# Kernel tuning notes

Hardware: AMD Instinct MI355X
Metric: run time of the kernel (lower is better)

The kernel has to match this reference:

```python
import jax, jax.numpy as jnp
import numpy as np

N = 100000
E = 3200000
F_IN = 256
F_OUT = 256
HID = 64


def setup_inputs() -> dict:
    key = jax.random.key(0)
    ks = jax.random.split(key, 16)
    stdv = 1.0 / np.sqrt(F_OUT)
    std_att = 1.0 / np.sqrt(HID)
    std_att_vec = 1.0 / np.sqrt(3.0)
    u = lambda k, shape, s: jax.random.uniform(k, shape, jnp.float32, -s, s)
    return {
        "inputx": jax.random.normal(ks[0], (N, F_IN), jnp.float32),
        "row_A": jax.random.randint(ks[1], (E,), 0, N),
        "col_A": jax.random.randint(ks[2], (E,), 0, N),
        "val_A": jax.random.uniform(ks[3], (E,), jnp.float32),
        "row_A2": jax.random.randint(ks[4], (E,), 0, N),
        "col_A2": jax.random.randint(ks[5], (E,), 0, N),
        "val_A2": jax.random.uniform(ks[6], (E,), jnp.float32),
        "weight_A": u(ks[7], (F_IN, F_OUT), stdv),
        "weight_A2": u(ks[8], (F_IN, F_OUT), stdv),
        "weight_mlp": u(ks[9], (F_IN, F_OUT), stdv),
        "W_k0": u(ks[10], (F_OUT, HID), std_att),
        "W_k1": u(ks[11], (F_OUT, HID), std_att),
        "W_k2": u(ks[12], (F_OUT, HID), std_att),
        "att_vec_A": u(ks[13], (F_OUT, HID), std_att),
        "att_vec_A2": u(ks[14], (F_OUT, HID), std_att),
        "att_vec_mlp": u(ks[15], (F_OUT, HID), std_att),
        "att_vec": u(jax.random.fold_in(key, 99), (3, 3), std_att_vec),
    }


def _spmm(row, col, val, x, n):
    # COO sparse-dense matmul: out[r] += val_e * x[c]
    return jax.ops.segment_sum(val[:, None] * x[col], row, num_segments=n)


def reference(inputx, row_A, col_A, val_A, row_A2, col_A2, val_A2,
              weight_A, weight_A2, weight_mlp, W_k0, W_k1, W_k2,
              att_vec_A, att_vec_A2, att_vec_mlp, att_vec):
    n = inputx.shape[0]
    out_A = jax.nn.relu(_spmm(row_A, col_A, val_A, inputx @ weight_A, n))
    out_A2 = jax.nn.relu(_spmm(row_A2, col_A2, val_A2, inputx @ weight_A2, n))
    out_mlp = jax.nn.relu(inputx @ weight_mlp)
    # attention gating
    T = 3.0
    k0 = jnp.mean(out_A @ W_k0, axis=0, keepdims=True)    # [1, HID]
    k1 = jnp.mean(out_A2 @ W_k1, axis=0, keepdims=True)
    k2 = jnp.mean(out_mlp @ W_k2, axis=0, keepdims=True)
    logits = jnp.concatenate([
        (out_A @ att_vec_A) @ k0.T,      # [N, 1]
        (out_A2 @ att_vec_A2) @ k1.T,
        (out_mlp @ att_vec_mlp) @ k2.T,
    ], axis=1)                           # [N, 3]
    att = jax.nn.softmax((jax.nn.sigmoid(logits) @ att_vec) / T, axis=1)
    return 3.0 * (att[:, 0:1] * out_A + att[:, 1:2] * out_A2 + att[:, 2:3] * out_mlp)
```

## Files before the change

### kernel.cpp

```cpp
#include <hip/hip_runtime.h>

typedef __bf16 bf16;
typedef __bf16 bf16x4 __attribute__((ext_vector_type(4)));
typedef __bf16 bf16x8 __attribute__((ext_vector_type(8)));
typedef float f32x4 __attribute__((ext_vector_type(4)));

__device__ __forceinline__ f32x4 bf2f(bf16x4 v){
  f32x4 r; r[0]=(float)v[0]; r[1]=(float)v[1]; r[2]=(float)v[2]; r[3]=(float)v[3]; return r;
}

#define RB    256
#define NBMAX 400
#define NBP   401
#define CHUNK 8192
#define CAP   9216

__global__ __launch_bounds__(256) void k_xcvt(const float* __restrict__ X, bf16* __restrict__ Xb, int total){
  int i = (blockIdx.x*256 + threadIdx.x)*8;
  if (i + 8 <= total){
    float4 a = *(const float4*)(X+i);
    float4 b = *(const float4*)(X+i+4);
    bf16x8 v;
    v[0]=(bf16)a.x; v[1]=(bf16)a.y; v[2]=(bf16)a.z; v[3]=(bf16)a.w;
    v[4]=(bf16)b.x; v[5]=(bf16)b.y; v[6]=(bf16)b.z; v[7]=(bf16)b.w;
    *(bf16x8*)(Xb+i) = v;
  }
}

__global__ __launch_bounds__(256) void k_wt(const float* __restrict__ W0, const float* __restrict__ W1,
                                            const float* __restrict__ W2, bf16* __restrict__ WT3){
  int n = blockIdx.x, mat = blockIdx.y, k = threadIdx.x;
  const float* W = (mat==0)?W0:((mat==1)?W1:W2);
  WT3[mat*65536 + n*256 + k] = (bf16)W[k*256 + n];
}

__global__ __launch_bounds__(512) void k_binT(const int* __restrict__ rowA, const int* __restrict__ colA,
    const float* __restrict__ valA, const int* __restrict__ rowA2, const int* __restrict__ colA2,
    const float* __restrict__ valA2, int* __restrict__ gcur,
    int2* __restrict__ pTA, int2* __restrict__ pTA2, int E, int NB){
  __shared__ int hist[NBMAX];
  __shared__ int lstart[NBMAX];
  __shared__ int delta[NBMAX];
  __shared__ int ss[512];
  __shared__ unsigned short sidx[CHUNK];
  __shared__ unsigned short bop[CHUNK];
  int mat = blockIdx.y;
  const int* row = mat? rowA2 : rowA;
  const int* col = mat? colA2 : colA;
  const float* val = mat? valA2 : valA;
  int2* pT = mat? pTA2 : pTA;
  int t = threadIdx.x;
  for (int i=t; i<NB; i+=512) hist[i] = 0;
  __syncthreads();
  int base = blockIdx.x * CHUNK;
  int endi = base + CHUNK; if (endi > E) endi = E;
  int cnt = endi - base;
  for (int i = base + t; i < endi; i += 512) atomicAdd(&hist[row[i] >> 8], 1);
  __syncthreads();
  int v = (t < NB) ? hist[t] : 0;
  ss[t] = v; __syncthreads();
  for (int off=1; off<512; off<<=1){
    int u = (t>=off)? ss[t-off] : 0;
    __syncthreads();
    ss[t] += u;
    __syncthreads();
  }
  if (t < NB){
    int excl = ss[t] - v;
    lstart[t] = excl;
    int ofs = v ? atomicAdd(&gcur[mat*NB + t], v) : 0;
    if (ofs > CAP - v) ofs = (CAP - v > 0) ? CAP - v : 0;
    delta[t] = (t*CAP + ofs) - excl;
    hist[t] = 0;
  }
  __syncthreads();
  for (int i = base + t; i < endi; i += 512){
    int b = row[i] >> 8;
    int lpos = lstart[b] + atomicAdd(&hist[b], 1);
    sidx[lpos] = (unsigned short)(i - base);
    bop[lpos]  = (unsigned short)b;
  }
  __syncthreads();
  for (int j = t; j < cnt; j += 512){
    int i = base + (int)sidx[j];
    int b = bop[j];
    int r = row[i];
    int2 p; p.x = ((r & 255) << 17) | col[i]; p.y = __float_as_int(val[i]);
    pT[delta[b] + j] = p;
  }
}

__global__ __launch_bounds__(256) void k_bscan(const int* __restrict__ gcur, int* __restrict__ gstart,
    int NB, int E){
  __shared__ int ss[256];
  __shared__ int carry;
  int mat = blockIdx.x;
  int t = threadIdx.x;
  if (t==0) carry = 0;
  __syncthreads();
  for (int base=0; base<NB; base+=256){
    int i = base + t;
    int v = (i < NB) ? gcur[mat*NB + i] : 0;
    ss[t] = v; __syncthreads();
    for (int off=1; off<256; off<<=1){
      int u = (t>=off)? ss[t-off] : 0;
      __syncthreads();
      ss[t] += u;
      __syncthreads();
    }
    int excl = carry + ss[t] - v;
    if (i < NB) gstart[mat*NBP + i] = excl;
    int tot = ss[255];
    __syncthreads();
    if (t==0) carry += tot;
    __syncthreads();
  }
  if (t==0) gstart[mat*NBP + NB] = E;
}

__global__ __launch_bounds__(512) void k_csr(const int2* __restrict__ pTA, const int2* __restrict__ pTA2,
    const int* __restrict__ gcur, const int* __restrict__ gstart,
    int* __restrict__ rsA, int* __restrict__ rsA2,
    int2* __restrict__ permA, int2* __restrict__ permA2, int N, int NB, int E){
  __shared__ unsigned short sidx[CAP];
  __shared__ int fill[RB];
  __shared__ int rowst[RB];
  __shared__ int ss[512];
  int mat = blockIdx.y;
  const int2* pT = mat? pTA2 : pTA;
  int2* perm = mat? permA2 : permA;
  int* rs = mat? rsA2 : rsA;
  int b = blockIdx.x;
  int t = threadIdx.x;
  int r0 = b*RB;
  int src = b*CAP;
  int cnt = gcur[mat*NB + b];
  if (cnt > CAP) cnt = CAP;
  int dst = gstart[mat*NBP + b];
  if (t < RB) fill[t] = 0;
  __syncthreads();
  for (int i = t; i < cnt; i += 512) atomicAdd(&fill[pT[src + i].x >> 17], 1);
  __syncthreads();
  int v = (t < RB) ? fill[t] : 0;
  ss[t] = v; __syncthreads();
  for (int off=1; off<512; off<<=1){
    int u = (t>=off)? ss[t-off] : 0;
    __syncthreads();
    ss[t] += u;
    __syncthreads();
  }
  if (t < RB){
    int excl = ss[t] - v;
    rowst[t] = excl;
    if (r0 + t < N) rs[r0 + t] = dst + excl;
    fill[t] = 0;
  }
  __syncthreads();
  for (int i = t; i < cnt; i += 512){
    int rl = pT[src + i].x >> 17;
    int lp = rowst[rl] + atomicAdd(&fill[rl], 1);
    sidx[lp] = (unsigned short)i;
  }
  __syncthreads();
  for (int j = t; j < cnt; j += 512){
    int2 e = pT[src + (int)sidx[j]];
    int2 o; o.x = e.x & 0x1FFFF; o.y = e.y;
    perm[dst + j] = o;
  }
  if (t == 0 && b == NB-1) rs[N] = E;
}

__global__ __launch_bounds__(256) void k_spmm(const bf16* __restrict__ Xb,
    const int* __restrict__ rsA, const int* __restrict__ rsA2,
    const int2* __restrict__ permA, const int2* __restrict__ permA2,
    bf16* __restrict__ AXb, bf16* __restrict__ A2Xb, int N){
  int mat = blockIdx.y;
  const int* rs = mat? rsA2 : rsA;
  const int2* perm = mat? permA2 : permA;
  bf16* dst = mat? A2Xb : AXb;
  int t = threadIdx.x, lane = t & 63, wv = t >> 6;
  int c = lane*4;
  int rstep = gridDim.x*4;

  for (int row = blockIdx.x*4 + wv; row < N; row += rstep){
    int e = rs[row], eend = rs[row+1];
    f32x4 acc; acc[0]=0.f; acc[1]=0.f; acc[2]=0.f; acc[3]=0.f;

    int2 p0, p1, p2, p3;
    bool have = (e + 3 < eend);
    if (have){ p0 = perm[e]; p1 = perm[e+1]; p2 = perm[e+2]; p3 = perm[e+3]; }
    while (have){
      bf16x4 g0 = *(const bf16x4*)(Xb + (size_t)p0.x*256 + c);
      bf16x4 g1 = *(const bf16x4*)(Xb + (size_t)p1.x*256 + c);
      bf16x4 g2 = *(const bf16x4*)(Xb + (size_t)p2.x*256 + c);
      bf16x4 g3 = *(const bf16x4*)(Xb + (size_t)p3.x*256 + c);
      float v0 = __int_as_float(p0.y), v1 = __int_as_float(p1.y);
      float v2 = __int_as_float(p2.y), v3 = __int_as_float(p3.y);
      e += 4;
      have = (e + 3 < eend);
      if (have){ p0 = perm[e]; p1 = perm[e+1]; p2 = perm[e+2]; p3 = perm[e+3]; }
      acc += v0 * bf2f(g0);
      acc += v1 * bf2f(g1);
      acc += v2 * bf2f(g2);
      acc += v3 * bf2f(g3);
    }
    for (; e < eend; ++e){
      int2 p = perm[e];
      acc += __int_as_float(p.y) * bf2f(*(const bf16x4*)(Xb + (size_t)p.x*256 + c));
    }
    bf16x4 o;
#pragma unroll
    for (int k=0;k<4;k++) o[k] = (bf16)acc[k];
    *(bf16x4*)(dst + (size_t)row*256 + c) = o;
  }
}

__global__ __launch_bounds__(512) void k_gemm(bf16* __restrict__ M0, bf16* __restrict__ M1,
        bf16* __restrict__ M2, const bf16* __restrict__ WT3, float* __restrict__ colsum, int N){
  __shared__ __align__(16) bf16 sA[128*32];
  __shared__ __align__(16) bf16 sB[256*32];
  __shared__ float gcs[256];
  int t = threadIdx.x;
  int lane = t & 63, wave = t>>6, wm = wave>>2, wn = wave&3;
  int mat = blockIdx.y;
  int m0 = blockIdx.x*128;
  const bf16* WT = WT3 + mat*65536;
  bf16* M = (mat==0)?M0:((mat==1)?M1:M2);

  f32x4 acc[4][4];
#pragma unroll
  for (int i=0;i<4;i++)
#pragma unroll
    for (int j=0;j<4;j++){ acc[i][j][0]=0.f; acc[i][j][1]=0.f; acc[i][j][2]=0.f; acc[i][j][3]=0.f; }

  int ar = t>>2, ac = t&3;
  int alc = ac ^ ((ar>>1)&3);
  int agrow = m0 + ar; if (agrow > N-1) agrow = N-1;
  const bf16* gA = M + (size_t)agrow*256 + alc*8;
  bf16* lA = sA + ar*32 + ac*8;

  int br = t>>2, bc = t&3;
  int blc = bc ^ ((br>>1)&3);
  const bf16* gB0 = WT + br*256 + blc*8;
  const bf16* gB1 = WT + (br+128)*256 + blc*8;
  bf16* lB0 = sB + br*32 + bc*8;
  bf16* lB1 = sB + (br+128)*32 + bc*8;

  for (int k0=0; k0<256; k0+=32){
    __syncthreads();
    *(bf16x8*)lA  = *(const bf16x8*)(gA  + k0);
    *(bf16x8*)lB0 = *(const bf16x8*)(gB0 + k0);
    *(bf16x8*)lB1 = *(const bf16x8*)(gB1 + k0);
    __syncthreads();

    bf16x8 af[4], bfr[4];
#pragma unroll
    for (int i=0;i<4;i++){
      int arow = wm*64 + i*16 + (lane&15);
      int pc = (lane>>4) ^ ((arow>>1)&3);
      af[i] = *(const bf16x8*)(sA + arow*32 + pc*8);
    }
#pragma unroll
    for (int j=0;j<4;j++){
      int brow = wn*64 + j*16 + (lane&15);
      int pc = (lane>>4) ^ ((brow>>1)&3);
      bfr[j] = *(const bf16x8*)(sB + brow*32 + pc*8);
    }
#pragma unroll
    for (int i=0;i<4;i++)
#pragma unroll
      for (int j=0;j<4;j++)
        acc[i][j] = __builtin_amdgcn_mfma_f32_16x16x32_bf16(af[i], bfr[j], acc[i][j], 0,0,0);
  }

  int col0 = wn*64 + (lane&15);
  int rb = m0 + wm*64 + ((lane>>4)<<2);
  float pj[4] = {0.f,0.f,0.f,0.f};
#pragma unroll
  for (int i=0;i<4;i++){
#pragma unroll
    for (int tt=0; tt<4; tt++){
      int r = rb + i*16 + tt;
      if (r < N){
#pragma unroll
        for (int j=0;j<4;j++){
          float vv = acc[i][j][tt];
          if (vv < 0.f) vv = 0.f;
          pj[j] += vv;
          M[(size_t)r*256 + col0 + j*16] = (bf16)vv;
        }
      }
    }
  }
  if (t < 256) gcs[t] = 0.f;
  __syncthreads();
#pragma unroll
  for (int j=0;j<4;j++) atomicAdd(&gcs[col0 + j*16], pj[j]);
  __syncthreads();
  if (t < 256) atomicAdd(&colsum[mat*256 + t], gcs[t]);
}

__global__ void k_attn(const float* __restrict__ colsum,
    const float* __restrict__ Wk0, const float* __restrict__ Wk1, const float* __restrict__ Wk2,
    const float* __restrict__ V0, const float* __restrict__ V1, const float* __restrict__ V2,
    float* __restrict__ wvec, int N){
  __shared__ float smean[768];
  __shared__ float sk[192];
  int t = threadIdx.x;
  float invN = 1.f/(float)N;
  smean[t]     = colsum[t]     * invN;
  smean[t+256] = colsum[t+256] * invN;
  smean[t+512] = colsum[t+512] * invN;
  __syncthreads();
  if (t < 192){
    int j = t>>6, h = t&63;
    const float* Wk = (j==0)?Wk0:((j==1)?Wk1:Wk2);
    float s = 0.f;
    for (int cc=0; cc<256; cc++) s += smean[j*256+cc]*Wk[cc*64+h];
    sk[j*64+h] = s;
  }
  __syncthreads();
  int c = t;
  for (int j=0;j<3;j++){
    const float* V = (j==0)?V0:((j==1)?V1:V2);
    float s = 0.f;
    for (int h=0;h<64;h++) s += V[c*64+h]*sk[j*64+h];
    wvec[j*256+c] = s;
  }
}

__global__ __launch_bounds__(256) void k_epi(const bf16* __restrict__ A, const bf16* __restrict__ B,
    const bf16* __restrict__ M, const float* __restrict__ wvec, const float* __restrict__ av9,
    float* __restrict__ out, int N){
  __shared__ float sw[768];
  __shared__ float sav[9];
  int t = threadIdx.x;
  sw[t] = wvec[t]; sw[t+256] = wvec[t+256]; sw[t+512] = wvec[t+512];
  if (t < 9) sav[t] = av9[t];
  __syncthreads();
  int row = blockIdx.x*4 + (t>>6);
  if (row >= N) return;
  int lane = t & 63;
  int c = lane*4;
  f32x4 a = bf2f(*(const bf16x4*)(A + (size_t)row*256 + c));
  f32x4 b = bf2f(*(const bf16x4*)(B + (size_t)row*256 + c));
  f32x4 m = bf2f(*(const bf16x4*)(M + (size_t)row*256 + c));
  float p0 = a[0]*sw[c] + a[1]*sw[c+1] + a[2]*sw[c+2] + a[3]*sw[c+3];
  float p1 = b[0]*sw[256+c] + b[1]*sw[256+c+1] + b[2]*sw[256+c+2] + b[3]*sw[256+c+3];
  float p2 = m[0]*sw[512+c] + m[1]*sw[512+c+1] + m[2]*sw[512+c+2] + m[3]*sw[512+c+3];
#pragma unroll
  for (int off=32; off>=1; off>>=1){
    p0 += __shfl_xor(p0, off);
    p1 += __shfl_xor(p1, off);
    p2 += __shfl_xor(p2, off);
  }
  float s0 = 1.f/(1.f+expf(-p0));
  float s1 = 1.f/(1.f+expf(-p1));
  float s2 = 1.f/(1.f+expf(-p2));
  float g0 = (s0*sav[0] + s1*sav[3] + s2*sav[6]) * (1.f/3.f);
  float g1 = (s0*sav[1] + s1*sav[4] + s2*sav[7]) * (1.f/3.f);
  float g2 = (s0*sav[2] + s1*sav[5] + s2*sav[8]) * (1.f/3.f);
  float mx = fmaxf(g0, fmaxf(g1,g2));
  float e0 = expf(g0-mx), e1 = expf(g1-mx), e2 = expf(g2-mx);
  float inv = 3.f/(e0+e1+e2);
  float a0 = e0*inv, a1 = e1*inv, a2 = e2*inv;
  f32x4 o = a0*a + a1*b + a2*m;
  *(f32x4*)(out + (size_t)row*256 + c) = o;
}

extern "C" void kernel_launch(void* const* d_in, const int* in_sizes, int n_in,
                              void* d_out, int out_size, void* d_ws, size_t ws_size,
                              hipStream_t stream){
  const float* X    = (const float*)d_in[0];
  const int*   rowA = (const int*)d_in[1];
  const int*   colA = (const int*)d_in[2];
  const float* valA = (const float*)d_in[3];
  const int*   rowA2= (const int*)d_in[4];
  const int*   colA2= (const int*)d_in[5];
  const float* valA2= (const float*)d_in[6];
  const float* W0   = (const float*)d_in[7];
  const float* W1   = (const float*)d_in[8];
  const float* W2   = (const float*)d_in[9];
  const float* Wk0  = (const float*)d_in[10];
  const float* Wk1  = (const float*)d_in[11];
  const float* Wk2  = (const float*)d_in[12];
  const float* V0   = (const float*)d_in[13];
  const float* V1   = (const float*)d_in[14];
  const float* V2   = (const float*)d_in[15];
  const float* AV9  = (const float*)d_in[16];
  int N = in_sizes[0] / 256;
  int E = in_sizes[1];
  int NB = (N + RB-1) >> 8;
  int ebl = (E + CHUNK-1)/CHUNK;

  char* ws = (char*)d_ws;
  size_t off = 0;
  auto take = [&](size_t b)->char*{ char* r = ws + off; off = (off + b + 255) & ~(size_t)255; return r; };
  size_t mb = (size_t)N*256*2;
  bf16* WT3  = (bf16*)take((size_t)3*256*256*2);
  bf16* Xb   = (bf16*)take(mb);
  bf16* B1   = (bf16*)take(mb);
  bf16* B2   = (bf16*)take(mb);
  int* rsA    = (int*)take((size_t)(N+1)*4);
  int* rsA2   = (int*)take((size_t)(N+1)*4);
  int* gcur   = (int*)take((size_t)2*NB*4);
  int* gstart = (int*)take((size_t)2*NBP*4);
  float* colsum = (float*)take(768*4);
  float* wvec   = (float*)take(768*4);
  int2* permA  = (int2*)take((size_t)E*8);
  int2* permA2 = (int2*)take((size_t)E*8);
  int2* pTA  = (int2*)B1;
  int2* pTA2 = (int2*)B2;

  hipMemsetAsync(gcur, 0, (size_t)2*NB*4, stream);
  hipMemsetAsync(colsum, 0, 768*4, stream);

  int total = N*256;
  k_xcvt<<<dim3((total/8 + 255)/256),256,0,stream>>>(X, Xb, total);
  k_wt<<<dim3(256,3),256,0,stream>>>(W0,W1,W2,WT3);
  k_binT<<<dim3(ebl,2),512,0,stream>>>(rowA,colA,valA,rowA2,colA2,valA2,gcur,pTA,pTA2,E,NB);
  k_bscan<<<2,256,0,stream>>>(gcur,gstart,NB,E);
  k_csr<<<dim3(NB,2),512,0,stream>>>(pTA,pTA2,gcur,gstart,rsA,rsA2,permA,permA2,N,NB,E);
  int sblk = (N+31)/32;
  k_spmm<<<dim3(sblk,2),256,0,stream>>>(Xb,rsA,rsA2,permA,permA2,B1,B2,N);
  k_gemm<<<dim3((N+127)/128,3),512,0,stream>>>(B1,B2,Xb,WT3,colsum,N);
  k_attn<<<1,256,0,stream>>>(colsum,Wk0,Wk1,Wk2,V0,V1,V2,wvec,N);
  k_epi<<<dim3((N+3)/4),256,0,stream>>>(B1,B2,Xb,wvec,AV9,(float*)d_out,N);
}
```

Baseline: 1.019 ms.

## Fuse preprocessing kernels and memsets, fold bucket scan into CSR build

```diff
diff --git a/kernel.cpp b/kernel.cpp
--- a/kernel.cpp
+++ b/kernel.cpp
@@ -11,27 +11,33 @@
 
 #define RB    256
 #define NBMAX 400
-#define NBP   401
 #define CHUNK 8192
 #define CAP   9216
 
-__global__ __launch_bounds__(256) void k_xcvt(const float* __restrict__ X, bf16* __restrict__ Xb, int total){
-  int i = (blockIdx.x*256 + threadIdx.x)*8;
-  if (i + 8 <= total){
-    float4 a = *(const float4*)(X+i);
-    float4 b = *(const float4*)(X+i+4);
-    bf16x8 v;
-    v[0]=(bf16)a.x; v[1]=(bf16)a.y; v[2]=(bf16)a.z; v[3]=(bf16)a.w;
-    v[4]=(bf16)b.x; v[5]=(bf16)b.y; v[6]=(bf16)b.z; v[7]=(bf16)b.w;
-    *(bf16x8*)(Xb+i) = v;
-  }
-}
-
-__global__ __launch_bounds__(256) void k_wt(const float* __restrict__ W0, const float* __restrict__ W1,
-                                            const float* __restrict__ W2, bf16* __restrict__ WT3){
-  int n = blockIdx.x, mat = blockIdx.y, k = threadIdx.x;
-  const float* W = (mat==0)?W0:((mat==1)?W1:W2);
-  WT3[mat*65536 + n*256 + k] = (bf16)W[k*256 + n];
+__global__ __launch_bounds__(256) void k_pre(const float* __restrict__ X, bf16* __restrict__ Xb, int total,
+    const float* __restrict__ W0, const float* __restrict__ W1, const float* __restrict__ W2,
+    bf16* __restrict__ WT3, int* __restrict__ gcur, float* __restrict__ colsum, int NB){
+  int b = blockIdx.x, t = threadIdx.x;
+  int nx = (total/8 + 255)/256;
+  if (b < nx){
+    int i = (b*256 + t)*8;
+    if (i + 8 <= total){
+      float4 a = *(const float4*)(X+i);
+      float4 c = *(const float4*)(X+i+4);
+      bf16x8 v;
+      v[0]=(bf16)a.x; v[1]=(bf16)a.y; v[2]=(bf16)a.z; v[3]=(bf16)a.w;
+      v[4]=(bf16)c.x; v[5]=(bf16)c.y; v[6]=(bf16)c.z; v[7]=(bf16)c.w;
+      *(bf16x8*)(Xb+i) = v;
+    }
+  } else if (b < nx + 768){
+    int wb = b - nx;
+    int mat = wb >> 8, n = wb & 255, k = t;
+    const float* W = (mat==0)?W0:((mat==1)?W1:W2);
+    WT3[mat*65536 + n*256 + k] = (bf16)W[k*256 + n];
+  } else {
+    for (int i=t; i<2*NB; i+=256) gcur[i] = 0;
+    colsum[t] = 0.f; colsum[t+256] = 0.f; colsum[t+512] = 0.f;
+  }
 }
 
 __global__ __launch_bounds__(512) void k_binT(const int* __restrict__ rowA, const int* __restrict__ colA,
@@ -90,39 +96,11 @@
   }
 }
 
-__global__ __launch_bounds__(256) void k_bscan(const int* __restrict__ gcur, int* __restrict__ gstart,
-    int NB, int E){
-  __shared__ int ss[256];
-  __shared__ int carry;
-  int mat = blockIdx.x;
-  int t = threadIdx.x;
-  if (t==0) carry = 0;
-  __syncthreads();
-  for (int base=0; base<NB; base+=256){
-    int i = base + t;
-    int v = (i < NB) ? gcur[mat*NB + i] : 0;
-    ss[t] = v; __syncthreads();
-    for (int off=1; off<256; off<<=1){
-      int u = (t>=off)? ss[t-off] : 0;
-      __syncthreads();
-      ss[t] += u;
-      __syncthreads();
-    }
-    int excl = carry + ss[t] - v;
-    if (i < NB) gstart[mat*NBP + i] = excl;
-    int tot = ss[255];
-    __syncthreads();
-    if (t==0) carry += tot;
-    __syncthreads();
-  }
-  if (t==0) gstart[mat*NBP + NB] = E;
-}
-
 __global__ __launch_bounds__(512) void k_csr(const int2* __restrict__ pTA, const int2* __restrict__ pTA2,
-    const int* __restrict__ gcur, const int* __restrict__ gstart,
-    int* __restrict__ rsA, int* __restrict__ rsA2,
+    const int* __restrict__ gcur, int* __restrict__ rsA, int* __restrict__ rsA2,
     int2* __restrict__ permA, int2* __restrict__ permA2, int N, int NB, int E){
   __shared__ unsigned short sidx[CAP];
+  __shared__ unsigned char key8[CAP];
   __shared__ int fill[RB];
   __shared__ int rowst[RB];
   __shared__ int ss[512];
@@ -134,12 +112,24 @@
   int t = threadIdx.x;
   int r0 = b*RB;
   int src = b*CAP;
-  int cnt = gcur[mat*NB + b];
-  if (cnt > CAP) cnt = CAP;
-  int dst = gstart[mat*NBP + b];
+  const int* gc = gcur + mat*NB;
+  int part = 0;
+  for (int i = t; i < b; i += 512) part += gc[i];
+  ss[t] = part; __syncthreads();
+  for (int off=256; off>=1; off>>=1){
+    if (t < off) ss[t] += ss[t+off];
+    __syncthreads();
+  }
+  int dst = ss[0];
+  int cnt = gc[b]; if (cnt > CAP) cnt = CAP;
+  __syncthreads();
   if (t < RB) fill[t] = 0;
   __syncthreads();
-  for (int i = t; i < cnt; i += 512) atomicAdd(&fill[pT[src + i].x >> 17], 1);
+  for (int i = t; i < cnt; i += 512){
+    int rl = pT[src + i].x >> 17;
+    key8[i] = (unsigned char)rl;
+    atomicAdd(&fill[rl], 1);
+  }
   __syncthreads();
   int v = (t < RB) ? fill[t] : 0;
   ss[t] = v; __syncthreads();
@@ -157,7 +147,7 @@
   }
   __syncthreads();
   for (int i = t; i < cnt; i += 512){
-    int rl = pT[src + i].x >> 17;
+    int rl = key8[i];
     int lp = rowst[rl] + atomicAdd(&fill[rl], 1);
     sidx[lp] = (unsigned short)i;
   }
@@ -404,7 +394,6 @@
   int* rsA    = (int*)take((size_t)(N+1)*4);
   int* rsA2   = (int*)take((size_t)(N+1)*4);
   int* gcur   = (int*)take((size_t)2*NB*4);
-  int* gstart = (int*)take((size_t)2*NBP*4);
   float* colsum = (float*)take(768*4);
   float* wvec   = (float*)take(768*4);
   int2* permA  = (int2*)take((size_t)E*8);
@@ -412,15 +401,11 @@
   int2* pTA  = (int2*)B1;
   int2* pTA2 = (int2*)B2;
 
-  hipMemsetAsync(gcur, 0, (size_t)2*NB*4, stream);
-  hipMemsetAsync(colsum, 0, 768*4, stream);
-
   int total = N*256;
-  k_xcvt<<<dim3((total/8 + 255)/256),256,0,stream>>>(X, Xb, total);
-  k_wt<<<dim3(256,3),256,0,stream>>>(W0,W1,W2,WT3);
+  int nx = (total/8 + 255)/256;
+  k_pre<<<dim3(nx + 768 + 1),256,0,stream>>>(X, Xb, total, W0,W1,W2, WT3, gcur, colsum, NB);
   k_binT<<<dim3(ebl,2),512,0,stream>>>(rowA,colA,valA,rowA2,colA2,valA2,gcur,pTA,pTA2,E,NB);
-  k_bscan<<<2,256,0,stream>>>(gcur,gstart,NB,E);
-  k_csr<<<dim3(NB,2),512,0,stream>>>(pTA,pTA2,gcur,gstart,rsA,rsA2,permA,permA2,N,NB,E);
+  k_csr<<<dim3(NB,2),512,0,stream>>>(pTA,pTA2,gcur,rsA,rsA2,permA,permA2,N,NB,E);
   int sblk = (N+31)/32;
   k_spmm<<<dim3(sblk,2),256,0,stream>>>(Xb,rsA,rsA2,permA,permA2,B1,B2,N);
   k_gemm<<<dim3((N+127)/128,3),512,0,stream>>>(B1,B2,Xb,WT3,colsum,N);
```

After: 1.004 ms. About the same (-1.5%).
